# Kernel optimization log

Measured on AMD Instinct MI355X. Metric: run time of the kernel, lower is better.

Reference implementation:

```python
import jax, jax.numpy as jnp
import numpy as np

EPS = 1e-6

def _rms_norm(x, w):
    # normalize over last dim (head_dim)
    var = jnp.mean(jnp.square(x), axis=-1, keepdims=True)
    return x * jax.lax.rsqrt(var + EPS) * w

def _rotate_half(x):
    half = x.shape[-1] // 2
    first, second = x[..., :half], x[..., half:]
    return jnp.concatenate([-second, first], axis=-1)

def _apply_rope(x, cos, sin):
    # x: [B,H,S,D]; cos/sin: [B,S,D] -> broadcast over heads
    return x * cos[:, None] + _rotate_half(x) * sin[:, None]

def setup_inputs() -> dict:
    key = jax.random.key(0)
    ks = jax.random.split(key, 10)
    B, Sq, Sk, Dm, H = 2, 2048, 2048, 2048, 16
    hd = Dm // H
    scale = 1.0 / np.sqrt(Dm)
    return {
        "x": jax.random.normal(ks[0], (B, Sq, Dm), jnp.float32),
        "context": jax.random.normal(ks[1], (B, Sk, Dm), jnp.float32),
        "cos_q": jax.random.uniform(ks[2], (B, Sq, hd), jnp.float32),
        "sin_q": jax.random.uniform(ks[3], (B, Sq, hd), jnp.float32),
        "cos_k": jax.random.uniform(ks[4], (B, Sk, hd), jnp.float32),
        "sin_k": jax.random.uniform(ks[5], (B, Sk, hd), jnp.float32),
        "Wq": jax.random.normal(ks[6], (Dm, Dm), jnp.float32) * scale,
        "Wk": jax.random.normal(ks[7], (Dm, Dm), jnp.float32) * scale,
        "Wv": jax.random.normal(ks[8], (Dm, Dm), jnp.float32) * scale,
        "Wo": jax.random.normal(ks[9], (Dm, Dm), jnp.float32) * scale,
        "q_norm_w": jnp.ones((hd,), jnp.float32),
        "k_norm_w": jnp.ones((hd,), jnp.float32),
    }

def reference(x, context, cos_q, sin_q, cos_k, sin_k, Wq, Wk, Wv, Wo, q_norm_w, k_norm_w):
    B, Sq, Dm = x.shape
    hd = q_norm_w.shape[0]
    H = Dm // hd
    # projections (torch Linear: y = x @ W.T), reshape to [B,H,S,D]
    q = (x @ Wq.T).reshape(B, Sq, H, hd).transpose(0, 2, 1, 3)
    k = (context @ Wk.T).reshape(B, -1, H, hd).transpose(0, 2, 1, 3)
    v = (context @ Wv.T).reshape(B, -1, H, hd).transpose(0, 2, 1, 3)
    # per-head QK RMSNorm
    q = _rms_norm(q, q_norm_w)
    k = _rms_norm(k, k_norm_w)
    # RoPE
    q = _apply_rope(q, cos_q, sin_q)
    k = _apply_rope(k, cos_k, sin_k)
    # SDPA, scale = 1/sqrt(head_dim)
    scale = 1.0 / np.sqrt(hd).astype(np.float32)
    scores = jnp.einsum('bhqd,bhkd->bhqk', q, k) * scale
    attn = jax.nn.softmax(scores, axis=-1)
    y = jnp.einsum('bhqk,bhkd->bhqd', attn, v)
    y = y.transpose(0, 2, 1, 3).reshape(B, Sq, Dm)
    return y @ Wo.T
```

## Files before the change

### kernel.cpp

```cpp
#include <hip/hip_runtime.h>


typedef __attribute__((ext_vector_type(8))) short bf16x8;
typedef __attribute__((ext_vector_type(4))) float f32x4;

#define AS1(p) ((__attribute__((address_space(1))) void*)(p))
#define AS3(p) ((__attribute__((address_space(3))) void*)(p))

__device__ __forceinline__ unsigned short f2bf(float f) {
  unsigned int u = __float_as_uint(f);
  u += 0x7fffu + ((u >> 16) & 1u);
  return (unsigned short)(u >> 16);
}
__device__ __forceinline__ float bf2f(unsigned short u) {
  return __uint_as_float(((unsigned int)u) << 16);
}

constexpr int B_ = 2, S_ = 2048, DM = 2048, H_ = 16, HD = 128;
constexpr int M_ = B_ * S_;

__global__ __launch_bounds__(256) void castbf(const float* __restrict__ X,
                                              unsigned short* __restrict__ Y, int n4) {
  int i = blockIdx.x * 256 + threadIdx.x;
  if (i >= n4) return;
  float4 v = ((const float4*)X)[i];
  ushort4 u;
  u.x = f2bf(v.x); u.y = f2bf(v.y); u.z = f2bf(v.z); u.w = f2bf(v.w);
  ((ushort4*)Y)[i] = u;
}

template <int BF16OUT>
__device__ __forceinline__ void gemm_core(const unsigned short* __restrict__ A,
                                          const unsigned short* __restrict__ Bw,
                                          void* __restrict__ Cv,
                                          unsigned short* lA, unsigned short* lB) {
  const int tid = threadIdx.x, wave = tid >> 6, lane = tid & 63;
  const int quad = lane >> 4, l16 = lane & 15;
  const int m0 = blockIdx.x * 256, n0 = blockIdx.y * 128;
  const int wm = (wave >> 1) * 64, wn = (wave & 1) * 64;
  constexpr int NT = DM / 32;

  f32x4 acc[4][4];
#pragma unroll
  for (int i = 0; i < 4; i++)
#pragma unroll
    for (int j = 0; j < 4; j++) acc[i][j] = (f32x4){0.f, 0.f, 0.f, 0.f};

  const int c0 = wave * 64 + lane;
  const int rA0 = c0 >> 2, dA0 = (c0 & 3) ^ ((rA0 >> 1) & 3);
  const int c1 = 512 + c0;
  const int rA1 = c1 >> 2, dA1 = (c1 & 3) ^ ((rA1 >> 1) & 3);
  const unsigned short* gA0 = A + (size_t)(m0 + rA0) * DM + dA0 * 8;
  const unsigned short* gA1 = A + (size_t)(m0 + rA1) * DM + dA1 * 8;
  const unsigned short* gB  = Bw + (size_t)(n0 + rA0) * DM + dA0 * 8;
  const int wdst = wave * 512;

#define STAGE(T)                                                                         \
  {                                                                                      \
    const int b_ = (T) & 3; const int k_ = (T) << 5;                                     \
    __builtin_amdgcn_global_load_lds(AS1(gA0 + k_), AS3(lA + b_ * 8192 + wdst), 16, 0, 0);\
    __builtin_amdgcn_global_load_lds(AS1(gA1 + k_), AS3(lA + b_ * 8192 + 4096 + wdst), 16, 0, 0);\
    __builtin_amdgcn_global_load_lds(AS1(gB + k_),  AS3(lB + b_ * 4096 + wdst), 16, 0, 0);\
  }

  STAGE(0) STAGE(1) STAGE(2)

  const int xoff = (quad ^ ((l16 >> 1) & 3)) * 8;

  for (int t = 0; t < NT; ++t) {
    if (t < NT - 2)       asm volatile("s_waitcnt vmcnt(6)\n\ts_barrier" ::: "memory");
    else if (t == NT - 2) asm volatile("s_waitcnt vmcnt(3)\n\ts_barrier" ::: "memory");
    else                  asm volatile("s_waitcnt vmcnt(0)\n\ts_barrier" ::: "memory");

    const unsigned short* ab = lA + (t & 3) * 8192;
    const unsigned short* bb = lB + (t & 3) * 4096;
    bf16x8 af[4], bf[4];
#pragma unroll
    for (int i = 0; i < 4; i++)
      af[i] = *(const bf16x8*)(ab + (wm + i * 16 + l16) * 32 + xoff);
#pragma unroll
    for (int j = 0; j < 4; j++)
      bf[j] = *(const bf16x8*)(bb + (wn + j * 16 + l16) * 32 + xoff);

    if (t + 3 < NT) STAGE(t + 3)

    __builtin_amdgcn_s_barrier();
    __builtin_amdgcn_s_setprio(1);
#pragma unroll
    for (int i = 0; i < 4; i++)
#pragma unroll
      for (int j = 0; j < 4; j++)
        acc[i][j] = __builtin_amdgcn_mfma_f32_16x16x32_bf16(af[i], bf[j], acc[i][j], 0, 0, 0);
    __builtin_amdgcn_s_setprio(0);
  }
#undef STAGE

#pragma unroll
  for (int i = 0; i < 4; i++)
#pragma unroll
    for (int j = 0; j < 4; j++) {
      const size_t row = (size_t)(m0 + wm + i * 16 + quad * 4);
      const int col = n0 + wn + j * 16 + l16;
      if (BF16OUT) {
        unsigned short* cp = (unsigned short*)Cv + row * DM + col;
#pragma unroll
        for (int r = 0; r < 4; r++) cp[(size_t)r * DM] = f2bf(acc[i][j][r]);
      } else {
        float* cp = (float*)Cv + row * DM + col;
#pragma unroll
        for (int r = 0; r < 4; r++) cp[(size_t)r * DM] = acc[i][j][r];
      }
    }
}

__global__ __launch_bounds__(512, 2) void gemm_qkv(const unsigned short* __restrict__ xb,
                                                   const unsigned short* __restrict__ cb,
                                                   const unsigned short* __restrict__ Wq,
                                                   const unsigned short* __restrict__ Wk,
                                                   const unsigned short* __restrict__ Wv,
                                                   unsigned short* __restrict__ Pq,
                                                   unsigned short* __restrict__ Pk,
                                                   unsigned short* __restrict__ Pv) {
  __shared__ __align__(16) unsigned short lA[4 * 8192];
  __shared__ __align__(16) unsigned short lB[4 * 4096];
  const int z = blockIdx.z;
  const unsigned short* A  = (z == 0) ? xb : cb;
  const unsigned short* Bw = (z == 0) ? Wq : (z == 1) ? Wk : Wv;
  unsigned short* C        = (z == 0) ? Pq : (z == 1) ? Pk : Pv;
  gemm_core<1>(A, Bw, C, lA, lB);
}

__global__ __launch_bounds__(512, 2) void gemm_bt(const unsigned short* __restrict__ A,
                                                  const unsigned short* __restrict__ Bw,
                                                  float* __restrict__ C) {
  __shared__ __align__(16) unsigned short lA[4 * 8192];
  __shared__ __align__(16) unsigned short lB[4 * 4096];
  gemm_core<0>(A, Bw, C, lA, lB);
}

__global__ __launch_bounds__(256) void normrope(const unsigned short* __restrict__ X,
                                                const float* __restrict__ Cs,
                                                const float* __restrict__ Sn,
                                                const float* __restrict__ W,
                                                unsigned short* __restrict__ Out,
                                                float scale) {
  int gw = (blockIdx.x * 256 + threadIdx.x) >> 6;
  int lane = threadIdx.x & 63;
  int h = gw & 15, bs = gw >> 4;
  int s = bs & (S_ - 1), b = bs >> 11;
  const unsigned short* xr = X + (size_t)gw * HD;
  float x0 = bf2f(xr[lane]), x1 = bf2f(xr[lane + 64]);
  float ss = x0 * x0 + x1 * x1;
#pragma unroll
  for (int off = 32; off > 0; off >>= 1) ss += __shfl_xor(ss, off);
  float rr = rsqrtf(ss * (1.0f / 128.0f) + 1e-6f);
  float n0 = x0 * rr * W[lane], n1 = x1 * rr * W[lane + 64];
  const float* cp = Cs + (size_t)bs * HD;
  const float* sp = Sn + (size_t)bs * HD;
  float o0 = (n0 * cp[lane] - n1 * sp[lane]) * scale;
  float o1 = (n1 * cp[lane + 64] + n0 * sp[lane + 64]) * scale;
  unsigned short* orow = Out + (((size_t)(b * H_ + h)) * S_ + s) * HD;
  orow[lane] = f2bf(o0);
  orow[lane + 64] = f2bf(o1);
}

__global__ __launch_bounds__(256) void vtrans(const unsigned short* __restrict__ Vf,
                                              unsigned short* __restrict__ Vt) {
  __shared__ unsigned short tile[128 * 72];
  const int tid = threadIdx.x;
  const int sc = blockIdx.x & 31;
  const int bh = blockIdx.x >> 5;
  const int b = bh >> 4, h = bh & 15;
  const int s0 = sc * 64;
#pragma unroll
  for (int it = 0; it < 4; ++it) {
    int ci = it * 256 + tid;
    int s = ci >> 4, dc = ci & 15;
    bf16x8 v = *(const bf16x8*)(Vf + ((size_t)(b * S_ + s0 + s)) * DM + h * HD + dc * 8);
    unsigned short* tp = tile + (dc * 8) * 72 + s;
#pragma unroll
    for (int e = 0; e < 8; e++) tp[e * 72] = (unsigned short)v[e];
  }
  __syncthreads();
#pragma unroll
  for (int it = 0; it < 4; ++it) {
    int cj = it * 256 + tid;
    int d = cj >> 3, scx = cj & 7;
    bf16x8 vv = *(const bf16x8*)(tile + d * 72 + scx * 8);
    *(bf16x8*)(Vt + ((size_t)bh * HD + d) * S_ + s0 + scx * 8) = vv;
  }
}

__global__ __launch_bounds__(128) void flash(const unsigned short* __restrict__ Q,
                                             const unsigned short* __restrict__ Kt,
                                             const unsigned short* __restrict__ Vt,
                                             unsigned short* __restrict__ Y) {
  __shared__ unsigned short lK[64 * HD];
  __shared__ unsigned short lV[HD * 64];
  __shared__ unsigned short lP[2 * 1024];
  const int tid = threadIdx.x, wave = tid >> 6, lane = tid & 63;
  const int quad = lane >> 4, l16 = lane & 15;
  const int qb = blockIdx.x & 31;
  const int bh = blockIdx.x >> 5;
  const int b = bh >> 4, h = bh & 15;
  const int q0 = qb * 64 + wave * 32;

  bf16x8 aq[2][4];
#pragma unroll
  for (int u = 0; u < 2; u++) {
    const unsigned short* qrow = Q + ((size_t)bh * S_ + q0 + u * 16 + l16) * HD;
#pragma unroll
    for (int t = 0; t < 4; t++) aq[u][t] = *(const bf16x8*)(qrow + t * 32 + quad * 8);
  }
  f32x4 o[2][8];
#pragma unroll
  for (int u = 0; u < 2; u++)
#pragma unroll
    for (int t = 0; t < 8; t++) o[u][t] = (f32x4){0.f, 0.f, 0.f, 0.f};
  float lsum[2][4] = {{0.f, 0.f, 0.f, 0.f}, {0.f, 0.f, 0.f, 0.f}};

  const unsigned short* kbase = Kt + (size_t)bh * S_ * HD;
  const unsigned short* vbase = Vt + (size_t)bh * HD * S_;
  unsigned short* lPw = lP + wave * 1024;
  const int mrow = quad * 4;
  const int xsl = (l16 >> 1) & 3;
  const int xsl7 = (l16 >> 1) & 7;

  for (int k0 = 0; k0 < S_; k0 += 64) {
    __syncthreads();
#pragma unroll
    for (int call = 0; call < 8; ++call) {
      int c = call * 128 + wave * 64 + lane;
      int key = c >> 4, sk = c & 15;
      int dck = sk ^ (key & 15);
      __builtin_amdgcn_global_load_lds(AS1(kbase + (size_t)(k0 + key) * HD + dck * 8),
                                       AS3(lK + (call * 128 + wave * 64) * 8), 16, 0, 0);
      int dv = c >> 3, sv = c & 7;
      int kc = sv ^ ((dv >> 1) & 7);
      __builtin_amdgcn_global_load_lds(AS1(vbase + (size_t)dv * S_ + k0 + kc * 8),
                                       AS3(lV + (call * 128 + wave * 64) * 8), 16, 0, 0);
    }
    __syncthreads();

#pragma unroll
    for (int h2 = 0; h2 < 2; ++h2) {
      f32x4 s0[2] = {(f32x4){0.f, 0.f, 0.f, 0.f}, (f32x4){0.f, 0.f, 0.f, 0.f}};
      f32x4 s1[2] = {(f32x4){0.f, 0.f, 0.f, 0.f}, (f32x4){0.f, 0.f, 0.f, 0.f}};
      {
        const unsigned short* krow0 = lK + (h2 * 32 + l16) * HD;
        const unsigned short* krow1 = krow0 + 16 * HD;
        __builtin_amdgcn_s_setprio(1);
#pragma unroll
        for (int t = 0; t < 4; t++) {
          int dcq = t * 4 + quad;
          bf16x8 kf0 = *(const bf16x8*)(krow0 + (dcq ^ l16) * 8);
          bf16x8 kf1 = *(const bf16x8*)(krow1 + (dcq ^ l16) * 8);
#pragma unroll
          for (int u = 0; u < 2; u++) {
            s0[u] = __builtin_amdgcn_mfma_f32_16x16x32_bf16(aq[u][t], kf0, s0[u], 0, 0, 0);
            s1[u] = __builtin_amdgcn_mfma_f32_16x16x32_bf16(aq[u][t], kf1, s1[u], 0, 0, 0);
          }
        }
        __builtin_amdgcn_s_setprio(0);
      }
#pragma unroll
      for (int u = 0; u < 2; u++) {
        unsigned short* lPu = lPw + u * 512;
#pragma unroll
        for (int r = 0; r < 4; r++) {
          int m = mrow + r;
          int sx = (m >> 1) & 3;
          float p0 = __expf(s0[u][r]);
          float p1 = __expf(s1[u][r]);
          lsum[u][r] += p0 + p1;
          int kc0 = l16 >> 3;
          lPu[m * 32 + ((kc0 ^ sx)) * 8 + (l16 & 7)] = f2bf(p0);
          lPu[m * 32 + (((kc0 + 2) ^ sx)) * 8 + (l16 & 7)] = f2bf(p1);
        }
      }
      bf16x8 pf[2];
#pragma unroll
      for (int u = 0; u < 2; u++)
        pf[u] = *(const bf16x8*)(lPw + u * 512 + l16 * 32 + (quad ^ xsl) * 8);
      __builtin_amdgcn_s_setprio(1);
#pragma unroll
      for (int t = 0; t < 8; t++) {
        bf16x8 vf = *(const bf16x8*)(lV + (t * 16 + l16) * 64 + ((h2 * 4 + quad) ^ xsl7) * 8);
#pragma unroll
        for (int u = 0; u < 2; u++)
          o[u][t] = __builtin_amdgcn_mfma_f32_16x16x32_bf16(pf[u], vf, o[u][t], 0, 0, 0);
      }
      __builtin_amdgcn_s_setprio(0);
    }
  }

#pragma unroll
  for (int off = 1; off < 16; off <<= 1) {
#pragma unroll
    for (int u = 0; u < 2; u++)
#pragma unroll
      for (int r = 0; r < 4; r++) lsum[u][r] += __shfl_xor(lsum[u][r], off);
  }
  float inv[2][4];
#pragma unroll
  for (int u = 0; u < 2; u++)
#pragma unroll
    for (int r = 0; r < 4; r++) inv[u][r] = 1.0f / lsum[u][r];
#pragma unroll
  for (int u = 0; u < 2; u++)
#pragma unroll
    for (int t = 0; t < 8; t++)
#pragma unroll
      for (int r = 0; r < 4; r++) {
        size_t idx = ((size_t)b * S_ + q0 + u * 16 + mrow + r) * DM + h * HD + t * 16 + l16;
        Y[idx] = f2bf(o[u][t][r] * inv[u][r]);
      }
}

extern "C" void kernel_launch(void* const* d_in, const int* in_sizes, int n_in,
                              void* d_out, int out_size, void* d_ws, size_t ws_size,
                              hipStream_t stream) {
  const float* x    = (const float*)d_in[0];
  const float* ctx  = (const float*)d_in[1];
  const float* cosq = (const float*)d_in[2];
  const float* sinq = (const float*)d_in[3];
  const float* cosk = (const float*)d_in[4];
  const float* sink = (const float*)d_in[5];
  const float* Wq   = (const float*)d_in[6];
  const float* Wk   = (const float*)d_in[7];
  const float* Wv   = (const float*)d_in[8];
  const float* Wo   = (const float*)d_in[9];
  const float* qw   = (const float*)d_in[10];
  const float* kw   = (const float*)d_in[11];

  char* ws = (char*)d_ws;
  const size_t ACT2 = (size_t)M_ * DM * 2;
  const size_t W2   = (size_t)DM * DM * 2;
  unsigned short* xb  = (unsigned short*)(ws);
  unsigned short* cb  = (unsigned short*)(ws + ACT2);
  unsigned short* Wqb = (unsigned short*)(ws + 2 * ACT2);
  unsigned short* Wkb = (unsigned short*)(ws + 2 * ACT2 + W2);
  unsigned short* Wvb = (unsigned short*)(ws + 2 * ACT2 + 2 * W2);
  unsigned short* Wob = (unsigned short*)(ws + 2 * ACT2 + 3 * W2);
  unsigned short* Pq  = (unsigned short*)(ws + 2 * ACT2 + 4 * W2);
  unsigned short* Pk  = (unsigned short*)(ws + 3 * ACT2 + 4 * W2);
  unsigned short* Pv  = (unsigned short*)(ws + 4 * ACT2 + 4 * W2);
  unsigned short* qn = xb;
  unsigned short* kn = Wqb;
  unsigned short* vt = cb;
  unsigned short* yb = Pq;

  const float scale = 0.0883883476483184f;

  castbf<<<M_ * DM / 1024, 256, 0, stream>>>(x, xb, M_ * DM / 4);
  castbf<<<M_ * DM / 1024, 256, 0, stream>>>(ctx, cb, M_ * DM / 4);
  castbf<<<DM * DM / 1024, 256, 0, stream>>>(Wq, Wqb, DM * DM / 4);
  castbf<<<DM * DM / 1024, 256, 0, stream>>>(Wk, Wkb, DM * DM / 4);
  castbf<<<DM * DM / 1024, 256, 0, stream>>>(Wv, Wvb, DM * DM / 4);
  castbf<<<DM * DM / 1024, 256, 0, stream>>>(Wo, Wob, DM * DM / 4);

  dim3 gq(M_ / 256, DM / 128, 3);
  gemm_qkv<<<gq, 512, 0, stream>>>(xb, cb, Wqb, Wkb, Wvb, Pq, Pk, Pv);

  normrope<<<M_ * H_ / 4, 256, 0, stream>>>(Pq, cosq, sinq, qw, qn, scale);
  normrope<<<M_ * H_ / 4, 256, 0, stream>>>(Pk, cosk, sink, kw, kn, 1.0f);
  vtrans<<<B_ * H_ * (S_ / 64), 256, 0, stream>>>(Pv, vt);

  flash<<<B_ * H_ * (S_ / 64), 128, 0, stream>>>(qn, kn, vt, yb);

  dim3 gg(M_ / 256, DM / 128);
  gemm_bt<<<gg, 512, 0, stream>>>(yb, Wob, (float*)d_out);

  (void)in_sizes; (void)n_in; (void)out_size; (void)ws_size;
}
```

Baseline: 489.3 us.

## Restructure GEMM core to K=64 tiles with triple-buffered split-phase loads

New measurement: 483.3 us. No clear change (-1.2%).

```diff
diff --git a/kernel.cpp b/kernel.cpp
--- a/kernel.cpp
+++ b/kernel.cpp
@@ -6,6 +6,7 @@
 
 #define AS1(p) ((__attribute__((address_space(1))) void*)(p))
 #define AS3(p) ((__attribute__((address_space(3))) void*)(p))
+#define STG(g, l) __builtin_amdgcn_global_load_lds(AS1(g), AS3(l), 16, 0, 0)
 
 __device__ __forceinline__ unsigned short f2bf(float f) {
   unsigned int u = __float_as_uint(f);
@@ -30,15 +31,16 @@
 }
 
 template <int BF16OUT>
-__device__ __forceinline__ void gemm_core(const unsigned short* __restrict__ A,
-                                          const unsigned short* __restrict__ Bw,
-                                          void* __restrict__ Cv,
-                                          unsigned short* lA, unsigned short* lB) {
+__device__ __forceinline__ void gemm8_core(const unsigned short* __restrict__ A,
+                                           const unsigned short* __restrict__ Bw,
+                                           void* __restrict__ Cv,
+                                           unsigned short* lds) {
   const int tid = threadIdx.x, wave = tid >> 6, lane = tid & 63;
   const int quad = lane >> 4, l16 = lane & 15;
   const int m0 = blockIdx.x * 256, n0 = blockIdx.y * 128;
   const int wm = (wave >> 1) * 64, wn = (wave & 1) * 64;
-  constexpr int NT = DM / 32;
+  constexpr int NT = DM / 64;
+  constexpr int SLOT = 24576;
 
   f32x4 acc[4][4];
 #pragma unroll
@@ -46,54 +48,86 @@
 #pragma unroll
     for (int j = 0; j < 4; j++) acc[i][j] = (f32x4){0.f, 0.f, 0.f, 0.f};
 
-  const int c0 = wave * 64 + lane;
-  const int rA0 = c0 >> 2, dA0 = (c0 & 3) ^ ((rA0 >> 1) & 3);
-  const int c1 = 512 + c0;
-  const int rA1 = c1 >> 2, dA1 = (c1 & 3) ^ ((rA1 >> 1) & 3);
-  const unsigned short* gA0 = A + (size_t)(m0 + rA0) * DM + dA0 * 8;
-  const unsigned short* gA1 = A + (size_t)(m0 + rA1) * DM + dA1 * 8;
-  const unsigned short* gB  = Bw + (size_t)(n0 + rA0) * DM + dA0 * 8;
-  const int wdst = wave * 512;
-
-#define STAGE(T)                                                                         \
-  {                                                                                      \
-    const int b_ = (T) & 3; const int k_ = (T) << 5;                                     \
-    __builtin_amdgcn_global_load_lds(AS1(gA0 + k_), AS3(lA + b_ * 8192 + wdst), 16, 0, 0);\
-    __builtin_amdgcn_global_load_lds(AS1(gA1 + k_), AS3(lA + b_ * 8192 + 4096 + wdst), 16, 0, 0);\
-    __builtin_amdgcn_global_load_lds(AS1(gB + k_),  AS3(lB + b_ * 4096 + wdst), 16, 0, 0);\
-  }
-
-  STAGE(0) STAGE(1) STAGE(2)
-
-  const int xoff = (quad ^ ((l16 >> 1) & 3)) * 8;
-
+  const int ch = ((tid & 7) ^ ((tid >> 3) & 7)) * 8;
+  const unsigned short* gA0 = A + (size_t)(m0 + (tid >> 3)) * DM + ch;
+  const unsigned short* gB0 = Bw + (size_t)(n0 + (tid >> 3)) * DM + ch;
+  const int wst = wave * 512;
+
+#define STG_H0(T, S)                                                          \
+  { const unsigned short* g_ = gA0 + (size_t)(T) * 64;                        \
+    STG(g_,          lds + (S) * SLOT + wst);                                 \
+    STG(g_ + 131072, lds + (S) * SLOT + 4096 + wst);                          \
+    STG(gB0 + (size_t)(T) * 64, lds + (S) * SLOT + 16384 + wst); }
+#define STG_H1(T, S)                                                          \
+  { const unsigned short* g_ = gA0 + (size_t)(T) * 64 + 262144;               \
+    STG(g_,          lds + (S) * SLOT + 8192 + wst);                          \
+    STG(g_ + 131072, lds + (S) * SLOT + 12288 + wst);                         \
+    STG(gB0 + (size_t)(T) * 64 + 131072,                                      \
+        lds + (S) * SLOT + 16384 + 4096 + wst); }
+
+  const int sx = (quad ^ (l16 & 7)) * 8;
+  const int aoff = (wm + l16) * 64;
+  const int boff = 16384 + (wn + l16) * 64;
+
+  STG_H0(0, 0) STG_H1(0, 0)
+  STG_H0(1, 1) STG_H1(1, 1)
+  asm volatile("s_waitcnt vmcnt(6)" ::: "memory");
+  __builtin_amdgcn_s_barrier();
+
+  int slot = 0;
   for (int t = 0; t < NT; ++t) {
-    if (t < NT - 2)       asm volatile("s_waitcnt vmcnt(6)\n\ts_barrier" ::: "memory");
-    else if (t == NT - 2) asm volatile("s_waitcnt vmcnt(3)\n\ts_barrier" ::: "memory");
-    else                  asm volatile("s_waitcnt vmcnt(0)\n\ts_barrier" ::: "memory");
-
-    const unsigned short* ab = lA + (t & 3) * 8192;
-    const unsigned short* bb = lB + (t & 3) * 4096;
-    bf16x8 af[4], bf[4];
-#pragma unroll
-    for (int i = 0; i < 4; i++)
-      af[i] = *(const bf16x8*)(ab + (wm + i * 16 + l16) * 32 + xoff);
-#pragma unroll
-    for (int j = 0; j < 4; j++)
-      bf[j] = *(const bf16x8*)(bb + (wn + j * 16 + l16) * 32 + xoff);
-
-    if (t + 3 < NT) STAGE(t + 3)
-
+    const unsigned short* ls = lds + slot * SLOT;
+    int s2 = slot + 2; if (s2 >= 3) s2 -= 3;
+
+    bf16x8 a0[2][2], bf[4][2];
+#pragma unroll
+    for (int i = 0; i < 2; i++) {
+      a0[i][0] = *(const bf16x8*)(ls + aoff + i * 1024 + sx);
+      a0[i][1] = *(const bf16x8*)(ls + aoff + i * 1024 + (sx ^ 32));
+    }
+#pragma unroll
+    for (int j = 0; j < 4; j++) {
+      bf[j][0] = *(const bf16x8*)(ls + boff + j * 1024 + sx);
+      bf[j][1] = *(const bf16x8*)(ls + boff + j * 1024 + (sx ^ 32));
+    }
+    if (t + 2 < NT) STG_H0(t + 2, s2)
     __builtin_amdgcn_s_barrier();
     __builtin_amdgcn_s_setprio(1);
 #pragma unroll
-    for (int i = 0; i < 4; i++)
-#pragma unroll
-      for (int j = 0; j < 4; j++)
-        acc[i][j] = __builtin_amdgcn_mfma_f32_16x16x32_bf16(af[i], bf[j], acc[i][j], 0, 0, 0);
+    for (int i = 0; i < 2; i++)
+#pragma unroll
+      for (int j = 0; j < 4; j++) {
+        acc[i][j] = __builtin_amdgcn_mfma_f32_16x16x32_bf16(a0[i][0], bf[j][0], acc[i][j], 0, 0, 0);
+        acc[i][j] = __builtin_amdgcn_mfma_f32_16x16x32_bf16(a0[i][1], bf[j][1], acc[i][j], 0, 0, 0);
+      }
     __builtin_amdgcn_s_setprio(0);
-  }
-#undef STAGE
+    __builtin_amdgcn_s_barrier();
+
+    bf16x8 a1[2][2];
+#pragma unroll
+    for (int i = 0; i < 2; i++) {
+      a1[i][0] = *(const bf16x8*)(ls + aoff + (i + 2) * 1024 + sx);
+      a1[i][1] = *(const bf16x8*)(ls + aoff + (i + 2) * 1024 + (sx ^ 32));
+    }
+    if (t + 2 < NT) STG_H1(t + 2, s2)
+    __builtin_amdgcn_s_barrier();
+    __builtin_amdgcn_s_setprio(1);
+#pragma unroll
+    for (int i = 0; i < 2; i++)
+#pragma unroll
+      for (int j = 0; j < 4; j++) {
+        acc[i + 2][j] = __builtin_amdgcn_mfma_f32_16x16x32_bf16(a1[i][0], bf[j][0], acc[i + 2][j], 0, 0, 0);
+        acc[i + 2][j] = __builtin_amdgcn_mfma_f32_16x16x32_bf16(a1[i][1], bf[j][1], acc[i + 2][j], 0, 0, 0);
+      }
+    __builtin_amdgcn_s_setprio(0);
+    if (t < NT - 2)       asm volatile("s_waitcnt vmcnt(6)" ::: "memory");
+    else if (t == NT - 2) asm volatile("s_waitcnt vmcnt(0)" ::: "memory");
+    __builtin_amdgcn_s_barrier();
+
+    slot++; if (slot == 3) slot = 0;
+  }
+#undef STG_H0
+#undef STG_H1
 
 #pragma unroll
   for (int i = 0; i < 4; i++)
@@ -121,21 +155,19 @@
                                                    unsigned short* __restrict__ Pq,
                                                    unsigned short* __restrict__ Pk,
                                                    unsigned short* __restrict__ Pv) {
-  __shared__ __align__(16) unsigned short lA[4 * 8192];
-  __shared__ __align__(16) unsigned short lB[4 * 4096];
+  __shared__ __align__(16) unsigned short lds[3 * 24576];
   const int z = blockIdx.z;
   const unsigned short* A  = (z == 0) ? xb : cb;
   const unsigned short* Bw = (z == 0) ? Wq : (z == 1) ? Wk : Wv;
   unsigned short* C        = (z == 0) ? Pq : (z == 1) ? Pk : Pv;
-  gemm_core<1>(A, Bw, C, lA, lB);
+  gemm8_core<1>(A, Bw, C, lds);
 }
 
 __global__ __launch_bounds__(512, 2) void gemm_bt(const unsigned short* __restrict__ A,
                                                   const unsigned short* __restrict__ Bw,
                                                   float* __restrict__ C) {
-  __shared__ __align__(16) unsigned short lA[4 * 8192];
-  __shared__ __align__(16) unsigned short lB[4 * 4096];
-  gemm_core<0>(A, Bw, C, lA, lB);
+  __shared__ __align__(16) unsigned short lds[3 * 24576];
+  gemm8_core<0>(A, Bw, C, lds);
 }
 
 __global__ __launch_bounds__(256) void normrope(const unsigned short* __restrict__ X,
```

## Restructure GEMM to 128x256 tiles with 4 waves and 3-stage LDS ring

Applied to the files above, without the earlier changes.

Result: faster. 478.1 us (-2.3%).

```diff
diff --git a/kernel.cpp b/kernel.cpp
--- a/kernel.cpp
+++ b/kernel.cpp
@@ -6,6 +6,7 @@
 
 #define AS1(p) ((__attribute__((address_space(1))) void*)(p))
 #define AS3(p) ((__attribute__((address_space(3))) void*)(p))
+#define STG(g, l) __builtin_amdgcn_global_load_lds(AS1(g), AS3(l), 16, 0, 0)
 
 __device__ __forceinline__ unsigned short f2bf(float f) {
   unsigned int u = __float_as_uint(f);
@@ -33,87 +34,100 @@
 __device__ __forceinline__ void gemm_core(const unsigned short* __restrict__ A,
                                           const unsigned short* __restrict__ Bw,
                                           void* __restrict__ Cv,
-                                          unsigned short* lA, unsigned short* lB) {
+                                          unsigned short* lds) {
   const int tid = threadIdx.x, wave = tid >> 6, lane = tid & 63;
   const int quad = lane >> 4, l16 = lane & 15;
-  const int m0 = blockIdx.x * 256, n0 = blockIdx.y * 128;
-  const int wm = (wave >> 1) * 64, wn = (wave & 1) * 64;
+  const int m0 = blockIdx.x * 128, n0 = blockIdx.y * 256;
+  const int wn = wave * 64;
   constexpr int NT = DM / 32;
-
-  f32x4 acc[4][4];
-#pragma unroll
-  for (int i = 0; i < 4; i++)
-#pragma unroll
-    for (int j = 0; j < 4; j++) acc[i][j] = (f32x4){0.f, 0.f, 0.f, 0.f};
-
-  const int c0 = wave * 64 + lane;
-  const int rA0 = c0 >> 2, dA0 = (c0 & 3) ^ ((rA0 >> 1) & 3);
-  const int c1 = 512 + c0;
-  const int rA1 = c1 >> 2, dA1 = (c1 & 3) ^ ((rA1 >> 1) & 3);
-  const unsigned short* gA0 = A + (size_t)(m0 + rA0) * DM + dA0 * 8;
-  const unsigned short* gA1 = A + (size_t)(m0 + rA1) * DM + dA1 * 8;
-  const unsigned short* gB  = Bw + (size_t)(n0 + rA0) * DM + dA0 * 8;
-  const int wdst = wave * 512;
-
-#define STAGE(T)                                                                         \
-  {                                                                                      \
-    const int b_ = (T) & 3; const int k_ = (T) << 5;                                     \
-    __builtin_amdgcn_global_load_lds(AS1(gA0 + k_), AS3(lA + b_ * 8192 + wdst), 16, 0, 0);\
-    __builtin_amdgcn_global_load_lds(AS1(gA1 + k_), AS3(lA + b_ * 8192 + 4096 + wdst), 16, 0, 0);\
-    __builtin_amdgcn_global_load_lds(AS1(gB + k_),  AS3(lB + b_ * 4096 + wdst), 16, 0, 0);\
-  }
-
-  STAGE(0) STAGE(1) STAGE(2)
-
-  const int xoff = (quad ^ ((l16 >> 1) & 3)) * 8;
-
+  constexpr int SLOT = 12288;
+
+  f32x4 acc[8][4];
+#pragma unroll
+  for (int f = 0; f < 8; f++)
+#pragma unroll
+    for (int g = 0; g < 4; g++) acc[f][g] = (f32x4){0.f, 0.f, 0.f, 0.f};
+
+  const unsigned short* srcA[2];
+  const unsigned short* srcB[4];
+#pragma unroll
+  for (int i = 0; i < 2; i++) {
+    int c = tid + i * 256, L = c >> 3, ph = c & 7, j = ph ^ (L & 7);
+    srcA[i] = A + (size_t)(m0 + L + ((j >> 2) << 6)) * DM + (j & 3) * 8;
+  }
+#pragma unroll
+  for (int i = 0; i < 4; i++) {
+    int c = tid + i * 256, L = c >> 3, ph = c & 7, j = ph ^ (L & 7);
+    srcB[i] = Bw + (size_t)(n0 + L + ((j >> 2) << 7)) * DM + (j & 3) * 8;
+  }
+
+#define STAGEK(T, S)                                                           \
+  { const int ko = (T) << 5; unsigned short* lb = lds + (S) * SLOT + wave * 512;\
+    STG(srcA[0] + ko, lb);                                                     \
+    STG(srcA[1] + ko, lb + 2048);                                              \
+    STG(srcB[0] + ko, lb + 4096);                                              \
+    STG(srcB[1] + ko, lb + 6144);                                              \
+    STG(srcB[2] + ko, lb + 8192);                                              \
+    STG(srcB[3] + ko, lb + 10240); }
+
+  const int x8 = l16 & 7;
+  const int ab0 = l16 * 64 + ((quad ^ x8)) * 8;
+  const int ab1 = l16 * 64 + (((4 | quad) ^ x8)) * 8;
+  const int bb  = 4096 + (wn & 64) * 64 + l16 * 64 +
+                  ((((wave >> 1) << 2) | quad) ^ x8) * 8;
+
+  STAGEK(0, 0) STAGEK(1, 1)
+  asm volatile("s_waitcnt vmcnt(6)" ::: "memory");
+  __builtin_amdgcn_s_barrier();
+
+  int st = 0, s2 = 2;
   for (int t = 0; t < NT; ++t) {
-    if (t < NT - 2)       asm volatile("s_waitcnt vmcnt(6)\n\ts_barrier" ::: "memory");
-    else if (t == NT - 2) asm volatile("s_waitcnt vmcnt(3)\n\ts_barrier" ::: "memory");
-    else                  asm volatile("s_waitcnt vmcnt(0)\n\ts_barrier" ::: "memory");
-
-    const unsigned short* ab = lA + (t & 3) * 8192;
-    const unsigned short* bb = lB + (t & 3) * 4096;
-    bf16x8 af[4], bf[4];
-#pragma unroll
-    for (int i = 0; i < 4; i++)
-      af[i] = *(const bf16x8*)(ab + (wm + i * 16 + l16) * 32 + xoff);
-#pragma unroll
-    for (int j = 0; j < 4; j++)
-      bf[j] = *(const bf16x8*)(bb + (wn + j * 16 + l16) * 32 + xoff);
-
-    if (t + 3 < NT) STAGE(t + 3)
-
-    __builtin_amdgcn_s_barrier();
+    const unsigned short* ls = lds + st * SLOT;
+    bf16x8 af[8], bfv[4];
+#pragma unroll
+    for (int f = 0; f < 4; f++) af[f]     = *(const bf16x8*)(ls + f * 1024 + ab0);
+#pragma unroll
+    for (int f = 0; f < 4; f++) af[f + 4] = *(const bf16x8*)(ls + f * 1024 + ab1);
+#pragma unroll
+    for (int g = 0; g < 4; g++) bfv[g]    = *(const bf16x8*)(ls + g * 1024 + bb);
+
+    if (t + 2 < NT) STAGEK(t + 2, s2)
+    if (t < NT - 2)       asm volatile("s_waitcnt vmcnt(6)" ::: "memory");
+    else if (t == NT - 2) asm volatile("s_waitcnt vmcnt(0)" ::: "memory");
+    if (t < NT - 1) __builtin_amdgcn_s_barrier();
+
     __builtin_amdgcn_s_setprio(1);
 #pragma unroll
-    for (int i = 0; i < 4; i++)
-#pragma unroll
-      for (int j = 0; j < 4; j++)
-        acc[i][j] = __builtin_amdgcn_mfma_f32_16x16x32_bf16(af[i], bf[j], acc[i][j], 0, 0, 0);
+    for (int f = 0; f < 8; f++)
+#pragma unroll
+      for (int g = 0; g < 4; g++)
+        acc[f][g] = __builtin_amdgcn_mfma_f32_16x16x32_bf16(af[f], bfv[g], acc[f][g], 0, 0, 0);
     __builtin_amdgcn_s_setprio(0);
-  }
-#undef STAGE
-
-#pragma unroll
-  for (int i = 0; i < 4; i++)
-#pragma unroll
-    for (int j = 0; j < 4; j++) {
-      const size_t row = (size_t)(m0 + wm + i * 16 + quad * 4);
-      const int col = n0 + wn + j * 16 + l16;
+
+    st++; if (st == 3) st = 0;
+    s2++; if (s2 == 3) s2 = 0;
+  }
+#undef STAGEK
+
+#pragma unroll
+  for (int f = 0; f < 8; f++)
+#pragma unroll
+    for (int g = 0; g < 4; g++) {
+      const size_t row = (size_t)(m0 + f * 16 + quad * 4);
+      const int col = n0 + wn + g * 16 + l16;
       if (BF16OUT) {
         unsigned short* cp = (unsigned short*)Cv + row * DM + col;
 #pragma unroll
-        for (int r = 0; r < 4; r++) cp[(size_t)r * DM] = f2bf(acc[i][j][r]);
+        for (int r = 0; r < 4; r++) cp[(size_t)r * DM] = f2bf(acc[f][g][r]);
       } else {
         float* cp = (float*)Cv + row * DM + col;
 #pragma unroll
-        for (int r = 0; r < 4; r++) cp[(size_t)r * DM] = acc[i][j][r];
+        for (int r = 0; r < 4; r++) cp[(size_t)r * DM] = acc[f][g][r];
       }
     }
 }
 
-__global__ __launch_bounds__(512, 2) void gemm_qkv(const unsigned short* __restrict__ xb,
+__global__ __launch_bounds__(256, 2) void gemm_qkv(const unsigned short* __restrict__ xb,
                                                    const unsigned short* __restrict__ cb,
                                                    const unsigned short* __restrict__ Wq,
                                                    const unsigned short* __restrict__ Wk,
@@ -121,21 +135,19 @@
                                                    unsigned short* __restrict__ Pq,
                                                    unsigned short* __restrict__ Pk,
                                                    unsigned short* __restrict__ Pv) {
-  __shared__ __align__(16) unsigned short lA[4 * 8192];
-  __shared__ __align__(16) unsigned short lB[4 * 4096];
+  __shared__ __align__(16) unsigned short lds[3 * 12288];
   const int z = blockIdx.z;
   const unsigned short* A  = (z == 0) ? xb : cb;
   const unsigned short* Bw = (z == 0) ? Wq : (z == 1) ? Wk : Wv;
   unsigned short* C        = (z == 0) ? Pq : (z == 1) ? Pk : Pv;
-  gemm_core<1>(A, Bw, C, lA, lB);
-}
-
-__global__ __launch_bounds__(512, 2) void gemm_bt(const unsigned short* __restrict__ A,
+  gemm_core<1>(A, Bw, C, lds);
+}
+
+__global__ __launch_bounds__(256, 2) void gemm_bt(const unsigned short* __restrict__ A,
                                                   const unsigned short* __restrict__ Bw,
                                                   float* __restrict__ C) {
-  __shared__ __align__(16) unsigned short lA[4 * 8192];
-  __shared__ __align__(16) unsigned short lB[4 * 4096];
-  gemm_core<0>(A, Bw, C, lA, lB);
+  __shared__ __align__(16) unsigned short lds[3 * 12288];
+  gemm_core<0>(A, Bw, C, lds);
 }
 
 __global__ __launch_bounds__(256) void normrope(const unsigned short* __restrict__ X,
@@ -359,8 +371,8 @@
   castbf<<<DM * DM / 1024, 256, 0, stream>>>(Wv, Wvb, DM * DM / 4);
   castbf<<<DM * DM / 1024, 256, 0, stream>>>(Wo, Wob, DM * DM / 4);
 
-  dim3 gq(M_ / 256, DM / 128, 3);
-  gemm_qkv<<<gq, 512, 0, stream>>>(xb, cb, Wqb, Wkb, Wvb, Pq, Pk, Pv);
+  dim3 gq(M_ / 128, DM / 256, 3);
+  gemm_qkv<<<gq, 256, 0, stream>>>(xb, cb, Wqb, Wkb, Wvb, Pq, Pk, Pv);
 
   normrope<<<M_ * H_ / 4, 256, 0, stream>>>(Pq, cosq, sinq, qw, qn, scale);
   normrope<<<M_ * H_ / 4, 256, 0, stream>>>(Pk, cosk, sink, kw, kn, 1.0f);
@@ -368,8 +380,8 @@
 
   flash<<<B_ * H_ * (S_ / 64), 128, 0, stream>>>(qn, kn, vt, yb);
 
-  dim3 gg(M_ / 256, DM / 128);
-  gemm_bt<<<gg, 512, 0, stream>>>(yb, Wob, (float*)d_out);
+  dim3 gg(M_ / 128, DM / 256);
+  gemm_bt<<<gg, 256, 0, stream>>>(yb, Wob, (float*)d_out);
 
   (void)in_sizes; (void)n_in; (void)out_size; (void)ws_size;
 }
```
